# Performance work log

Measured on AMD Instinct MI355X. Metric: run time of the kernel, lower is better.

## Reference

```python
import jax, jax.numpy as jnp
import numpy as np

NUM_HEADS = 16
HEAD_DIM = 64
ROPE_BASE = 160000.0


def _rope_tables(seq_len, head_dim):
    inv_freq = 1.0 / (ROPE_BASE ** (jnp.arange(0, head_dim, 2, dtype=jnp.float32) / head_dim))
    freqs = jnp.arange(seq_len, dtype=jnp.float32)[:, None] * inv_freq[None, :]  # [S, hd/2]
    return jnp.cos(freqs)[None, None], jnp.sin(freqs)[None, None]  # [1,1,S,hd/2]


def _apply_rope(x, cos, sin):
    # x: [B, nh, S, hd]; split-half rotation as in the torch module
    x1, x2 = jnp.split(x, 2, axis=-1)
    return jnp.concatenate([x1 * cos - x2 * sin, x2 * cos + x1 * sin], axis=-1)


def setup_inputs() -> dict:
    key = jax.random.key(0)
    k1, k2, k3 = jax.random.split(key, 3)
    B, S, H = 2, 2048, 1024
    hidden_states = jax.random.normal(k1, (B, S, H), dtype=jnp.float32)
    # additive causal mask: 0 for allowed, -1e9 for future positions
    causal = jnp.tril(jnp.ones((S, S), dtype=bool))
    attention_mask = jnp.where(causal, 0.0, -1e9).astype(jnp.float32)[None, None]
    Wqkv = jax.random.normal(k2, (H, 3 * H), dtype=jnp.float32) * (H ** -0.5)
    Wo = jax.random.normal(k3, (H, H), dtype=jnp.float32) * (H ** -0.5)
    return {"hidden_states": hidden_states, "attention_mask": attention_mask, "Wqkv": Wqkv, "Wo": Wo}


def reference(hidden_states, attention_mask, Wqkv, Wo):
    B, S, H = hidden_states.shape
    nh, hd = NUM_HEADS, HEAD_DIM
    scale = hd ** -0.5

    qkv = hidden_states @ Wqkv                                   # [B,S,3H]
    qkv = qkv.reshape(B, S, 3, nh, hd).transpose(2, 0, 3, 1, 4)  # [3,B,nh,S,hd]
    q, k, v = qkv[0], qkv[1], qkv[2]

    cos, sin = _rope_tables(S, hd)
    q = _apply_rope(q, cos, sin)
    k = _apply_rope(k, cos, sin)

    scores = jnp.einsum('bhqd,bhkd->bhqk', q, k) * scale + attention_mask
    attn = jax.nn.softmax(scores, axis=-1)
    out = jnp.einsum('bhqk,bhkd->bhqd', attn, v)                 # [B,nh,S,hd]
    out = out.transpose(0, 2, 1, 3).reshape(B, S, H)
    return out @ Wo
```

## Files before the change

### kernel.cpp

```cpp
#include <hip/hip_runtime.h>
#include <hip/hip_bf16.h>

typedef __bf16 bf16x8 __attribute__((ext_vector_type(8)));
typedef float f32x4 __attribute__((ext_vector_type(4)));
typedef unsigned short u16;

__device__ __forceinline__ u16 f2bf(float f) {
    union { float f; unsigned u; } x{f};
    unsigned r = x.u + 0x7fffu + ((x.u >> 16) & 1u);
    return (u16)(r >> 16);
}
__device__ __forceinline__ float bf2f(u16 h) {
    union { unsigned u; float f; } x{(unsigned)h << 16};
    return x.f;
}
__device__ __forceinline__ unsigned pk2(float a, float b) {
    union { float f; unsigned u; } x{a}, y{b};
    return ((x.u + 0x8000u) >> 16) | ((y.u + 0x8000u) & 0xffff0000u);
}
__device__ __forceinline__ float ex2(float x) { return __builtin_amdgcn_exp2f(x); }
__device__ __forceinline__ f32x4 zero4() { f32x4 z = {0.f, 0.f, 0.f, 0.f}; return z; }

typedef const __attribute__((address_space(1))) unsigned int* gp1_t;
typedef __attribute__((address_space(3))) unsigned int* lp3_t;
__device__ __forceinline__ void async16(const u16* g, u16* l) {
    __builtin_amdgcn_global_load_lds((gp1_t)g, (lp3_t)l, 16, 0, 0);
}

__global__ void __launch_bounds__(256) cast_bf16(const float* __restrict__ x,
                                                 u16* __restrict__ y, int n4) {
    int i = (blockIdx.x * 256 + threadIdx.x) * 4;
    if (i >= n4 * 4) return;
    float4 v = *(const float4*)(x + i);
    ushort4 o;
    o.x = f2bf(v.x); o.y = f2bf(v.y); o.z = f2bf(v.z); o.w = f2bf(v.w);
    *(ushort4*)(y + i) = o;
}

__global__ void __launch_bounds__(256) transpose_cast(const float* __restrict__ W,
                                                      u16* __restrict__ Wt, int K, int N) {
    __shared__ float tile[32][33];
    int tx = threadIdx.x, ty = threadIdx.y;
    int n0 = blockIdx.x * 32, k0 = blockIdx.y * 32;
#pragma unroll
    for (int i = 0; i < 32; i += 8)
        tile[ty + i][tx] = W[(size_t)(k0 + ty + i) * N + n0 + tx];
    __syncthreads();
#pragma unroll
    for (int i = 0; i < 32; i += 8)
        Wt[(size_t)(n0 + ty + i) * K + k0 + tx] = f2bf(tile[tx][ty + i]);
}

__global__ void __launch_bounds__(256) vtrans(const u16* __restrict__ qkv,
                                              u16* __restrict__ Vt) {
    __shared__ u16 tile[32][33];
    int tx = threadIdx.x, ty = threadIdx.y;
    int s0 = blockIdx.x * 32, d0 = blockIdx.y * 32;
    int bh = blockIdx.z, b = bh >> 4, h = bh & 15;
#pragma unroll
    for (int i = 0; i < 32; i += 8)
        tile[ty + i][tx] = qkv[((size_t)(b * 2048 + s0 + ty + i)) * 3072 + 2048 + h * 64 + d0 + tx];
    __syncthreads();
    size_t ob = (size_t)bh * 64 * 2048;
#pragma unroll
    for (int i = 0; i < 32; i += 8)
        Vt[ob + (size_t)(d0 + ty + i) * 2048 + s0 + tx] = tile[tx][ty + i];
}

template <typename OutT>
__global__ void __launch_bounds__(256) gemm_bt(const u16* __restrict__ A,
                                               const u16* __restrict__ Bt,
                                               OutT* __restrict__ C,
                                               int M, int N, int K) {
    __shared__ __align__(16) u16 As[128 * 32];
    __shared__ __align__(16) u16 Bs[128 * 32];
    const int t = threadIdx.x;
    const int lane = t & 63, w = t >> 6;
    const int wm = w >> 1, wn = w & 1;
    const int m16 = lane & 15, q4 = lane >> 4;
    const int bm = blockIdx.y, bn = blockIdx.x;

    const int lrow = lane >> 2;
    const int kchunk = (lane & 3) ^ ((lane >> 3) & 3);
    const u16* Ag = A + (size_t)(bm * 128 + w * 32 + lrow) * K + kchunk * 8;
    const u16* Bg = Bt + (size_t)(bn * 128 + w * 32 + lrow) * K + kchunk * 8;
    u16* Al0 = As + (w * 32) * 32;
    u16* Al1 = As + (w * 32 + 16) * 32;
    u16* Bl0 = Bs + (w * 32) * 32;
    u16* Bl1 = Bs + (w * 32 + 16) * 32;

    const int kswz = (q4 ^ ((m16 >> 1) & 3)) * 8;

    f32x4 acc[4][4];
#pragma unroll
    for (int i = 0; i < 4; i++)
#pragma unroll
        for (int j = 0; j < 4; j++) acc[i][j] = zero4();

    for (int k0 = 0; k0 < K; k0 += 32) {
        __syncthreads();
        async16(Ag + k0, Al0);
        async16(Ag + 16 * K + k0, Al1);
        async16(Bg + k0, Bl0);
        async16(Bg + 16 * K + k0, Bl1);
        __syncthreads();
        bf16x8 af[4], bf[4];
#pragma unroll
        for (int i = 0; i < 4; i++)
            af[i] = *(const bf16x8*)&As[(wm * 64 + i * 16 + m16) * 32 + kswz];
#pragma unroll
        for (int j = 0; j < 4; j++)
            bf[j] = *(const bf16x8*)&Bs[(wn * 64 + j * 16 + m16) * 32 + kswz];
#pragma unroll
        for (int i = 0; i < 4; i++)
#pragma unroll
            for (int j = 0; j < 4; j++)
                acc[i][j] = __builtin_amdgcn_mfma_f32_16x16x32_bf16(af[i], bf[j], acc[i][j], 0, 0, 0);
    }
#pragma unroll
    for (int i = 0; i < 4; i++)
#pragma unroll
        for (int j = 0; j < 4; j++)
#pragma unroll
            for (int rr = 0; rr < 4; rr++) {
                int row = bm * 128 + wm * 64 + i * 16 + q4 * 4 + rr;
                int col = bn * 128 + wn * 64 + j * 16 + m16;
                float v = acc[i][j][rr];
                if constexpr (sizeof(OutT) == 4) {
                    C[(size_t)row * N + col] = v;
                } else {
                    C[(size_t)row * N + col] = f2bf(v);
                }
            }
}

__global__ void __launch_bounds__(256) rope_kernel(const u16* __restrict__ qkv,
                                                   u16* __restrict__ Q,
                                                   u16* __restrict__ Kd) {
    int t = blockIdx.x * 256 + threadIdx.x;
    int d = t & 31;
    int h = (t >> 5) & 15;
    int s = (t >> 9) & 2047;
    int b = t >> 20;
    size_t in_base = ((size_t)(b * 2048 + s)) * 3072 + h * 64;
    float q1 = bf2f(qkv[in_base + d]);
    float q2 = bf2f(qkv[in_base + d + 32]);
    float k1 = bf2f(qkv[in_base + 1024 + d]);
    float k2 = bf2f(qkv[in_base + 1024 + d + 32]);

    const float c_log = 0.374466538f;
    float inv = expf(-(float)d * c_log);
    float th = (float)s * inv;
    float cs = cosf(th), sn = sinf(th);

    const float scale = 0.125f * 1.44269504f;
    size_t out_base = ((size_t)(b * 16 + h) * 2048 + s) * 64;
    Q[out_base + d]      = f2bf((q1 * cs - q2 * sn) * scale);
    Q[out_base + d + 32] = f2bf((q2 * cs + q1 * sn) * scale);
    Kd[out_base + d]      = f2bf(k1 * cs - k2 * sn);
    Kd[out_base + d + 32] = f2bf(k2 * cs + k1 * sn);
}

__global__ void __launch_bounds__(256) attn_kernel(const u16* __restrict__ Q,
                                                   const u16* __restrict__ Kg_,
                                                   const u16* __restrict__ Vtg_,
                                                   u16* __restrict__ O) {
    __shared__ __align__(16) u16 Ks[2][64][72];
    __shared__ __align__(16) u16 Vt[2][64][72];
    __shared__ __align__(16) u16 Pt[4][16][72];
    const int t = threadIdx.x, w = t >> 6;
    const int m16 = t & 15, q4 = (t & 63) >> 4;
    const int bx = blockIdx.x, bh = blockIdx.y;
    const size_t base = (size_t)bh * 2048 * 64;
    const int b = bh >> 4, h = bh & 15;
    const int skey = t >> 2, sc = (t & 3) * 16;

#pragma unroll 1
    for (int ph = 0; ph < 2; ph++) {
        const int qt = ph ? (31 - bx) : bx;
        const int qrow = qt * 64 + w * 16 + m16;
        const u16* Qg = Q + base + (size_t)qrow * 64;
        bf16x8 qf0 = *(const bf16x8*)(Qg + q4 * 8);
        bf16x8 qf1 = *(const bf16x8*)(Qg + 32 + q4 * 8);

        f32x4 occ[4];
#pragma unroll
        for (int dc = 0; dc < 4; dc++) occ[dc] = zero4();
        float li = 0.f;

        const u16* Kb0 = Kg_ + base + skey * 64 + sc;
        const u16* Vt0 = Vtg_ + base + (size_t)skey * 2048 + sc;
        uint4 ka = *(const uint4*)(Kb0);
        uint4 kb = *(const uint4*)(Kb0 + 8);
        uint4 va = *(const uint4*)(Vt0);
        uint4 vb = *(const uint4*)(Vt0 + 8);

#pragma unroll 1
        for (int jt = 0; jt <= qt; jt++) {
            const int bi = jt & 1;
            *(uint4*)&Ks[bi][skey][sc] = ka;
            *(uint4*)&Ks[bi][skey][sc + 8] = kb;
            *(uint4*)&Vt[bi][skey][sc] = va;
            *(uint4*)&Vt[bi][skey][sc + 8] = vb;
            if (jt < qt) {
                const u16* Kn = Kb0 + (size_t)(jt + 1) * 4096;
                const u16* Vn = Vt0 + (size_t)(jt + 1) * 64;
                ka = *(const uint4*)(Kn);
                kb = *(const uint4*)(Kn + 8);
                va = *(const uint4*)(Vn);
                vb = *(const uint4*)(Vn + 8);
            }
            __syncthreads();

            f32x4 st[4];
#pragma unroll
            for (int c = 0; c < 4; c++) st[c] = zero4();
#pragma unroll
            for (int c = 0; c < 4; c++) {
                bf16x8 kf0 = *(const bf16x8*)&Ks[bi][c * 16 + m16][q4 * 8];
                bf16x8 kf1 = *(const bf16x8*)&Ks[bi][c * 16 + m16][32 + q4 * 8];
                st[c] = __builtin_amdgcn_mfma_f32_16x16x32_bf16(kf0, qf0, st[c], 0, 0, 0);
                st[c] = __builtin_amdgcn_mfma_f32_16x16x32_bf16(kf1, qf1, st[c], 0, 0, 0);
            }

            float pv[4][4];
#pragma unroll
            for (int c = 0; c < 4; c++)
#pragma unroll
                for (int rr = 0; rr < 4; rr++) pv[c][rr] = st[c][rr];
            if (jt == qt) {
                const int ql = w * 16 + m16;
#pragma unroll
                for (int c = 0; c < 4; c++)
#pragma unroll
                    for (int rr = 0; rr < 4; rr++)
                        if (c * 16 + q4 * 4 + rr > ql) pv[c][rr] = -1e30f;
            }

#pragma unroll
            for (int c = 0; c < 4; c++) {
                float p0 = ex2(pv[c][0] - 24.f);
                float p1 = ex2(pv[c][1] - 24.f);
                float p2 = ex2(pv[c][2] - 24.f);
                float p3 = ex2(pv[c][3] - 24.f);
                li += (p0 + p1) + (p2 + p3);
                uint2 pkd = make_uint2(pk2(p0, p1), pk2(p2, p3));
                *(uint2*)&Pt[w][m16][c * 16 + q4 * 4] = pkd;
            }

#pragma unroll
            for (int ks = 0; ks < 2; ks++) {
                bf16x8 pf = *(const bf16x8*)&Pt[w][m16][ks * 32 + q4 * 8];
#pragma unroll
                for (int dc = 0; dc < 4; dc++) {
                    bf16x8 vf = *(const bf16x8*)&Vt[bi][dc * 16 + m16][ks * 32 + q4 * 8];
                    occ[dc] = __builtin_amdgcn_mfma_f32_16x16x32_bf16(vf, pf, occ[dc], 0, 0, 0);
                }
            }
        }

        li += __shfl_xor(li, 16);
        li += __shfl_xor(li, 32);
        float rli = 1.0f / li;
        u16* Op = O + ((size_t)(b * 2048 + qrow)) * 1024 + h * 64 + q4 * 4;
#pragma unroll
        for (int dc = 0; dc < 4; dc++) {
            ushort4 o;
            o.x = f2bf(occ[dc][0] * rli);
            o.y = f2bf(occ[dc][1] * rli);
            o.z = f2bf(occ[dc][2] * rli);
            o.w = f2bf(occ[dc][3] * rli);
            *(ushort4*)(Op + dc * 16) = o;
        }
        __syncthreads();
    }
}

extern "C" void kernel_launch(void* const* d_in, const int* in_sizes, int n_in,
                              void* d_out, int out_size, void* d_ws, size_t ws_size,
                              hipStream_t stream) {
    const float* hs   = (const float*)d_in[0];
    const float* Wqkv = (const float*)d_in[2];
    const float* Wo   = (const float*)d_in[3];
    float* out = (float*)d_out;

    const int BS = 4096;
    const int H = 1024, N3 = 3072;
    const int SH = 32 * 2048 * 64;

    u16* Xb    = (u16*)d_ws;
    u16* Wqkvt = Xb + (size_t)BS * H;
    u16* Wot   = Wqkvt + (size_t)N3 * H;
    u16* QKVb  = Wot + (size_t)H * H;
    u16* Qb    = QKVb + (size_t)BS * N3;
    u16* Kb    = Qb + SH;
    u16* Vtb   = Kb + SH;
    u16* AOb   = Vtb + SH;

    cast_bf16<<<(BS * H / 4 + 255) / 256, 256, 0, stream>>>(hs, Xb, BS * H / 4);
    transpose_cast<<<dim3(N3 / 32, H / 32), dim3(32, 8), 0, stream>>>(Wqkv, Wqkvt, H, N3);
    transpose_cast<<<dim3(H / 32, H / 32), dim3(32, 8), 0, stream>>>(Wo, Wot, H, H);

    gemm_bt<u16><<<dim3(N3 / 128, BS / 128), 256, 0, stream>>>(Xb, Wqkvt, QKVb, BS, N3, H);

    rope_kernel<<<(2 * 2048 * 16 * 32) / 256, 256, 0, stream>>>(QKVb, Qb, Kb);

    vtrans<<<dim3(64, 2, 32), dim3(32, 8), 0, stream>>>(QKVb, Vtb);

    attn_kernel<<<dim3(16, 32), 256, 0, stream>>>(Qb, Kb, Vtb, AOb);

    gemm_bt<float><<<dim3(H / 128, BS / 128), 256, 0, stream>>>(AOb, Wot, out, BS, H, H);
}
```

Baseline: 213.3 us.

## Fuse RoPE into QKV GEMM epilogue and merge prep kernels into one launch

Merges the input cast, both weight transposes and a new cos/sin table build into a single prep kernel. RoPE and the softmax scale are applied in the QKV GEMM epilogue, which writes Q, K and V directly in head-major layout, so the rope kernel and the bf16 QKV intermediate round trip go away. This removes launches and global traffic. In exchange the epilogue does scattered 2-byte stores and extra table loads, and vtrans still needs a separate pass over V.

```diff
diff --git a/kernel.cpp b/kernel.cpp
--- a/kernel.cpp
+++ b/kernel.cpp
@@ -10,10 +10,6 @@
     unsigned r = x.u + 0x7fffu + ((x.u >> 16) & 1u);
     return (u16)(r >> 16);
 }
-__device__ __forceinline__ float bf2f(u16 h) {
-    union { unsigned u; float f; } x{(unsigned)h << 16};
-    return x.f;
-}
 __device__ __forceinline__ unsigned pk2(float a, float b) {
     union { float f; unsigned u; } x{a}, y{b};
     return ((x.u + 0x8000u) >> 16) | ((y.u + 0x8000u) & 0xffff0000u);
@@ -27,50 +23,159 @@
     __builtin_amdgcn_global_load_lds((gp1_t)g, (lp3_t)l, 16, 0, 0);
 }
 
-__global__ void __launch_bounds__(256) cast_bf16(const float* __restrict__ x,
-                                                 u16* __restrict__ y, int n4) {
-    int i = (blockIdx.x * 256 + threadIdx.x) * 4;
-    if (i >= n4 * 4) return;
-    float4 v = *(const float4*)(x + i);
-    ushort4 o;
-    o.x = f2bf(v.x); o.y = f2bf(v.y); o.z = f2bf(v.z); o.w = f2bf(v.w);
-    *(ushort4*)(y + i) = o;
-}
-
-__global__ void __launch_bounds__(256) transpose_cast(const float* __restrict__ W,
-                                                      u16* __restrict__ Wt, int K, int N) {
+__global__ void __launch_bounds__(256) prep(const float* __restrict__ hs,
+                                            u16* __restrict__ Xb,
+                                            const float* __restrict__ Wqkv,
+                                            u16* __restrict__ Wqkvt,
+                                            const float* __restrict__ Wo,
+                                            u16* __restrict__ Wot,
+                                            float* __restrict__ cosT,
+                                            float* __restrict__ sinT) {
     __shared__ float tile[32][33];
-    int tx = threadIdx.x, ty = threadIdx.y;
-    int n0 = blockIdx.x * 32, k0 = blockIdx.y * 32;
-#pragma unroll
-    for (int i = 0; i < 32; i += 8)
-        tile[ty + i][tx] = W[(size_t)(k0 + ty + i) * N + n0 + tx];
-    __syncthreads();
-#pragma unroll
-    for (int i = 0; i < 32; i += 8)
-        Wt[(size_t)(n0 + ty + i) * K + k0 + tx] = f2bf(tile[tx][ty + i]);
-}
-
-__global__ void __launch_bounds__(256) vtrans(const u16* __restrict__ qkv,
+    const int blk = blockIdx.x, t = threadIdx.x;
+    if (blk < 4096) {
+        int i = (blk * 256 + t) * 4;
+        float4 v = *(const float4*)(hs + i);
+        ushort4 o;
+        o.x = f2bf(v.x); o.y = f2bf(v.y); o.z = f2bf(v.z); o.w = f2bf(v.w);
+        *(ushort4*)(Xb + i) = o;
+    } else if (blk < 8192) {
+        const float* W; u16* Wt; int N, bx, by;
+        if (blk < 7168) { int bid = blk - 4096; W = Wqkv; Wt = Wqkvt; N = 3072; bx = bid % 96; by = bid / 96; }
+        else            { int bid = blk - 7168; W = Wo;   Wt = Wot;   N = 1024; bx = bid % 32; by = bid / 32; }
+        const int K = 1024;
+        int tx = t & 31, ty = t >> 5;
+        int n0 = bx * 32, k0 = by * 32;
+#pragma unroll
+        for (int i = 0; i < 32; i += 8)
+            tile[ty + i][tx] = W[(size_t)(k0 + ty + i) * N + n0 + tx];
+        __syncthreads();
+#pragma unroll
+        for (int i = 0; i < 32; i += 8)
+            Wt[(size_t)(n0 + ty + i) * K + k0 + tx] = f2bf(tile[tx][ty + i]);
+    } else {
+        int idx = (blk - 8192) * 256 + t;
+        int d = idx & 31, s = idx >> 5;
+        float inv = expf(-(float)d * 0.374466538f);
+        float th = (float)s * inv;
+        cosT[idx] = cosf(th);
+        sinT[idx] = sinf(th);
+    }
+}
+
+__global__ void __launch_bounds__(256) vtrans(const u16* __restrict__ V,
                                               u16* __restrict__ Vt) {
     __shared__ u16 tile[32][33];
-    int tx = threadIdx.x, ty = threadIdx.y;
+    int t = threadIdx.x;
+    int tx = t & 31, ty = t >> 5;
     int s0 = blockIdx.x * 32, d0 = blockIdx.y * 32;
-    int bh = blockIdx.z, b = bh >> 4, h = bh & 15;
+    size_t bi = (size_t)blockIdx.z * 2048 * 64;
 #pragma unroll
     for (int i = 0; i < 32; i += 8)
-        tile[ty + i][tx] = qkv[((size_t)(b * 2048 + s0 + ty + i)) * 3072 + 2048 + h * 64 + d0 + tx];
+        tile[ty + i][tx] = V[bi + (size_t)(s0 + ty + i) * 64 + d0 + tx];
     __syncthreads();
-    size_t ob = (size_t)bh * 64 * 2048;
 #pragma unroll
     for (int i = 0; i < 32; i += 8)
-        Vt[ob + (size_t)(d0 + ty + i) * 2048 + s0 + tx] = tile[tx][ty + i];
-}
-
-template <typename OutT>
+        Vt[bi + (size_t)(d0 + ty + i) * 2048 + s0 + tx] = tile[tx][ty + i];
+}
+
+__global__ void __launch_bounds__(256) gemm_qkv(const u16* __restrict__ A,
+                                                const u16* __restrict__ Bt,
+                                                const float* __restrict__ cosT,
+                                                const float* __restrict__ sinT,
+                                                u16* __restrict__ Q,
+                                                u16* __restrict__ Kd,
+                                                u16* __restrict__ V) {
+    const int K = 1024, N = 3072;
+    __shared__ __align__(16) u16 As[128 * 32];
+    __shared__ __align__(16) u16 Bs[128 * 32];
+    const int t = threadIdx.x;
+    const int lane = t & 63, w = t >> 6;
+    const int wm = w >> 1, wn = w & 1;
+    const int m16 = lane & 15, q4 = lane >> 4;
+    const int bm = blockIdx.y, bn = blockIdx.x;
+
+    const int lrow = lane >> 2;
+    const int kchunk = (lane & 3) ^ ((lane >> 3) & 3);
+    const u16* Ag = A + (size_t)(bm * 128 + w * 32 + lrow) * K + kchunk * 8;
+    const u16* Bg = Bt + (size_t)(bn * 128 + w * 32 + lrow) * K + kchunk * 8;
+    u16* Al0 = As + (w * 32) * 32;
+    u16* Al1 = As + (w * 32 + 16) * 32;
+    u16* Bl0 = Bs + (w * 32) * 32;
+    u16* Bl1 = Bs + (w * 32 + 16) * 32;
+    const int kswz = (q4 ^ ((m16 >> 1) & 3)) * 8;
+
+    f32x4 acc[4][4];
+#pragma unroll
+    for (int i = 0; i < 4; i++)
+#pragma unroll
+        for (int j = 0; j < 4; j++) acc[i][j] = zero4();
+
+    for (int k0 = 0; k0 < K; k0 += 32) {
+        __syncthreads();
+        async16(Ag + k0, Al0);
+        async16(Ag + 16 * K + k0, Al1);
+        async16(Bg + k0, Bl0);
+        async16(Bg + 16 * K + k0, Bl1);
+        __syncthreads();
+        bf16x8 af[4], bf[4];
+#pragma unroll
+        for (int i = 0; i < 4; i++)
+            af[i] = *(const bf16x8*)&As[(wm * 64 + i * 16 + m16) * 32 + kswz];
+#pragma unroll
+        for (int j = 0; j < 4; j++)
+            bf[j] = *(const bf16x8*)&Bs[(wn * 64 + j * 16 + m16) * 32 + kswz];
+#pragma unroll
+        for (int i = 0; i < 4; i++)
+#pragma unroll
+            for (int j = 0; j < 4; j++)
+                acc[i][j] = __builtin_amdgcn_mfma_f32_16x16x32_bf16(af[i], bf[j], acc[i][j], 0, 0, 0);
+    }
+
+    const int colbase = bn * 128 + wn * 64;
+    const int type = colbase >> 10;
+    const int h = (colbase & 1023) >> 6;
+    const int rbase = bm * 128 + wm * 64;
+
+    if (type == 2) {
+#pragma unroll
+        for (int i = 0; i < 4; i++)
+#pragma unroll
+            for (int rr = 0; rr < 4; rr++) {
+                int r = rbase + i * 16 + q4 * 4 + rr;
+                int b = r >> 11, s = r & 2047;
+                size_t ob = ((size_t)((b * 16 + h) * 2048 + s)) * 64;
+#pragma unroll
+                for (int j = 0; j < 4; j++)
+                    V[ob + j * 16 + m16] = f2bf(acc[i][j][rr]);
+            }
+    } else {
+        u16* dst = (type == 0) ? Q : Kd;
+        const float qs = (type == 0) ? 0.1803368801f  : 1.0f;
+#pragma unroll
+        for (int i = 0; i < 4; i++)
+#pragma unroll
+            for (int rr = 0; rr < 4; rr++) {
+                int r = rbase + i * 16 + q4 * 4 + rr;
+                int b = r >> 11, s = r & 2047;
+                size_t ob = ((size_t)((b * 16 + h) * 2048 + s)) * 64;
+#pragma unroll
+                for (int j2 = 0; j2 < 2; j2++) {
+                    int d = j2 * 16 + m16;
+                    float cs = cosT[s * 32 + d];
+                    float sn = sinT[s * 32 + d];
+                    float x1 = acc[i][j2][rr];
+                    float x2 = acc[i][j2 + 2][rr];
+                    dst[ob + d]      = f2bf((x1 * cs - x2 * sn) * qs);
+                    dst[ob + d + 32] = f2bf((x2 * cs + x1 * sn) * qs);
+                }
+            }
+    }
+}
+
 __global__ void __launch_bounds__(256) gemm_bt(const u16* __restrict__ A,
                                                const u16* __restrict__ Bt,
-                                               OutT* __restrict__ C,
+                                               float* __restrict__ C,
                                                int M, int N, int K) {
     __shared__ __align__(16) u16 As[128 * 32];
     __shared__ __align__(16) u16 Bs[128 * 32];
@@ -88,7 +193,6 @@
     u16* Al1 = As + (w * 32 + 16) * 32;
     u16* Bl0 = Bs + (w * 32) * 32;
     u16* Bl1 = Bs + (w * 32 + 16) * 32;
-
     const int kswz = (q4 ^ ((m16 >> 1) & 3)) * 8;
 
     f32x4 acc[4][4];
@@ -125,40 +229,8 @@
             for (int rr = 0; rr < 4; rr++) {
                 int row = bm * 128 + wm * 64 + i * 16 + q4 * 4 + rr;
                 int col = bn * 128 + wn * 64 + j * 16 + m16;
-                float v = acc[i][j][rr];
-                if constexpr (sizeof(OutT) == 4) {
-                    C[(size_t)row * N + col] = v;
-                } else {
-                    C[(size_t)row * N + col] = f2bf(v);
-                }
-            }
-}
-
-__global__ void __launch_bounds__(256) rope_kernel(const u16* __restrict__ qkv,
-                                                   u16* __restrict__ Q,
-                                                   u16* __restrict__ Kd) {
-    int t = blockIdx.x * 256 + threadIdx.x;
-    int d = t & 31;
-    int h = (t >> 5) & 15;
-    int s = (t >> 9) & 2047;
-    int b = t >> 20;
-    size_t in_base = ((size_t)(b * 2048 + s)) * 3072 + h * 64;
-    float q1 = bf2f(qkv[in_base + d]);
-    float q2 = bf2f(qkv[in_base + d + 32]);
-    float k1 = bf2f(qkv[in_base + 1024 + d]);
-    float k2 = bf2f(qkv[in_base + 1024 + d + 32]);
-
-    const float c_log = 0.374466538f;
-    float inv = expf(-(float)d * c_log);
-    float th = (float)s * inv;
-    float cs = cosf(th), sn = sinf(th);
-
-    const float scale = 0.125f * 1.44269504f;
-    size_t out_base = ((size_t)(b * 16 + h) * 2048 + s) * 64;
-    Q[out_base + d]      = f2bf((q1 * cs - q2 * sn) * scale);
-    Q[out_base + d + 32] = f2bf((q2 * cs + q1 * sn) * scale);
-    Kd[out_base + d]      = f2bf(k1 * cs - k2 * sn);
-    Kd[out_base + d + 32] = f2bf(k2 * cs + k1 * sn);
+                C[(size_t)row * N + col] = acc[i][j][rr];
+            }
 }
 
 __global__ void __launch_bounds__(256) attn_kernel(const u16* __restrict__ Q,
@@ -291,23 +363,22 @@
     u16* Xb    = (u16*)d_ws;
     u16* Wqkvt = Xb + (size_t)BS * H;
     u16* Wot   = Wqkvt + (size_t)N3 * H;
-    u16* QKVb  = Wot + (size_t)H * H;
-    u16* Qb    = QKVb + (size_t)BS * N3;
+    u16* Qb    = Wot + (size_t)H * H;
     u16* Kb    = Qb + SH;
-    u16* Vtb   = Kb + SH;
+    u16* Vb    = Kb + SH;
+    u16* Vtb   = Vb + SH;
     u16* AOb   = Vtb + SH;
-
-    cast_bf16<<<(BS * H / 4 + 255) / 256, 256, 0, stream>>>(hs, Xb, BS * H / 4);
-    transpose_cast<<<dim3(N3 / 32, H / 32), dim3(32, 8), 0, stream>>>(Wqkv, Wqkvt, H, N3);
-    transpose_cast<<<dim3(H / 32, H / 32), dim3(32, 8), 0, stream>>>(Wo, Wot, H, H);
-
-    gemm_bt<u16><<<dim3(N3 / 128, BS / 128), 256, 0, stream>>>(Xb, Wqkvt, QKVb, BS, N3, H);
-
-    rope_kernel<<<(2 * 2048 * 16 * 32) / 256, 256, 0, stream>>>(QKVb, Qb, Kb);
-
-    vtrans<<<dim3(64, 2, 32), dim3(32, 8), 0, stream>>>(QKVb, Vtb);
+    float* cosT = (float*)(AOb + (size_t)BS * H);
+    float* sinT = cosT + 2048 * 32;
+
+    prep<<<8448, 256, 0, stream>>>(hs, Xb, Wqkv, Wqkvt, Wo, Wot, cosT, sinT);
+
+    gemm_qkv<<<dim3(N3 / 128, BS / 128), 256, 0, stream>>>(Xb, Wqkvt, cosT, sinT,
+                                                           Qb, Kb, Vb);
+
+    vtrans<<<dim3(64, 2, 32), 256, 0, stream>>>(Vb, Vtb);
 
     attn_kernel<<<dim3(16, 32), 256, 0, stream>>>(Qb, Kb, Vtb, AOb);
 
-    gemm_bt<float><<<dim3(H / 128, BS / 128), 256, 0, stream>>>(AOb, Wot, out, BS, H, H);
-}
+    gemm_bt<<<dim3(H / 128, BS / 128), 256, 0, stream>>>(AOb, Wot, out, BS, H, H);
+}
```

Result: no change. 210.9 us (-1.1%).
